# Kernel optimization log

Measured on AMD Instinct MI355X. Metric: run time of the kernel, lower is better.

The kernel has to match this reference:

```python
import jax, jax.numpy as jnp
import numpy as np

B, Q, S, T, H = 8, 64, 64, 64, 768
NH, HD = 12, 64  # head_num, head_dim


def setup_inputs() -> dict:
    key = jax.random.key(0)
    k1, k2, k3, k4, k5, k6, k7 = jax.random.split(key, 7)
    ini_q = jax.random.normal(k1, (B, Q, H), dtype=jnp.float32)
    ini_k = jax.random.normal(k2, (B, S, T, H), dtype=jnp.float32)
    mask = jax.random.randint(k3, (B, S, T), 0, 2).astype(jnp.float32)  # 1 = masked
    # learned params (Linear weights stored as [in, out] for x @ W)
    sc = 1.0 / np.sqrt(H)
    Wq = jax.random.normal(k4, (H, H), dtype=jnp.float32) * sc
    Wkv = jax.random.normal(k5, (H, H), dtype=jnp.float32) * sc
    Wo = jax.random.normal(k6, (H, H), dtype=jnp.float32) * sc
    bo = jax.random.normal(k7, (H,), dtype=jnp.float32) * 0.02
    return {"ini_q": ini_q, "ini_k": ini_k, "mask": mask,
            "Wq": Wq, "Wkv": Wkv, "Wo": Wo, "bo": bo}


def reference(ini_q, ini_k, mask, Wq, Wkv, Wo, bo):
    batch, q_num, _ = ini_q.shape
    _, s_num, t_num, _ = ini_k.shape
    scale = 1.0 / np.sqrt(HD)
    q = (ini_q @ Wq).reshape(batch, q_num, NH, HD)
    kv = (ini_k @ Wkv).reshape(batch, s_num, t_num, NH, HD)  # k == v
    # [b, h, q, s, t]
    scores = jnp.einsum('bqhd,bsthd->bhqst', q, kv) * scale
    scores = scores + mask[:, None, None, :, :] * -10000.0
    alpha = jax.nn.softmax(scores, axis=4)  # dropout is identity in eval
    res = jnp.einsum('bhqst,bsthd->bqshd', alpha, kv).reshape(batch, q_num, s_num, NH * HD)
    return res @ Wo + bo
```

## Files before the change

### kernel.cpp

```cpp
#include <hip/hip_runtime.h>
#include <stdint.h>


typedef __bf16 bf16_t;
typedef __attribute__((ext_vector_type(8))) __bf16 bf16x8;
typedef __attribute__((ext_vector_type(4))) __bf16 bf16x4;
typedef __attribute__((ext_vector_type(4))) float f32x4;

#define HDIM 768

__device__ __forceinline__ void gload16(const bf16_t* g, bf16_t* l) {
  __builtin_amdgcn_global_load_lds(
      (const __attribute__((address_space(1))) void*)g,
      (__attribute__((address_space(3))) void*)l, 16, 0, 0);
}

__global__ __launch_bounds__(256) void split4_kernel(const float* __restrict__ x,
                                                     bf16_t* __restrict__ h,
                                                     bf16_t* __restrict__ l) {
  const int i = blockIdx.x * 256 + threadIdx.x;
  const float4 v = ((const float4*)x)[i];
  const float vv[4] = {v.x, v.y, v.z, v.w};
  bf16x4 hv, lv;
#pragma unroll
  for (int e = 0; e < 4; ++e) {
    const bf16_t hb = (bf16_t)vv[e];
    hv[e] = hb;
    lv[e] = (bf16_t)(vv[e] - (float)hb);
  }
  ((bf16x4*)h)[i] = hv;
  ((bf16x4*)l)[i] = lv;
}

__global__ __launch_bounds__(256) void splitT3_kernel(
    const float* __restrict__ W0, const float* __restrict__ W1,
    const float* __restrict__ W2,
    bf16_t* __restrict__ h0, bf16_t* __restrict__ l0,
    bf16_t* __restrict__ h1, bf16_t* __restrict__ l1,
    bf16_t* __restrict__ h2, bf16_t* __restrict__ l2) {
  const int kt = blockIdx.x * 64, nt = blockIdx.y * 64, ws = blockIdx.z;
  const float* W = ws == 0 ? W0 : (ws == 1 ? W1 : W2);
  bf16_t* H = ws == 0 ? h0 : (ws == 1 ? h1 : h2);
  bf16_t* L = ws == 0 ? l0 : (ws == 1 ? l1 : l2);
  __shared__ bf16_t Th[64 * 72], Tl[64 * 72];
  const int tid = threadIdx.x;
  const int r0 = tid >> 4, c0 = (tid & 15) * 4;
#pragma unroll
  for (int rg = 0; rg < 4; ++rg) {
    const int r = r0 + rg * 16;
    const float4 v = *(const float4*)&W[(size_t)(kt + r) * HDIM + nt + c0];
    const float vv[4] = {v.x, v.y, v.z, v.w};
#pragma unroll
    for (int e = 0; e < 4; ++e) {
      const bf16_t hb = (bf16_t)vv[e];
      Th[(c0 + e) * 72 + r] = hb;
      Tl[(c0 + e) * 72 + r] = (bf16_t)(vv[e] - (float)hb);
    }
  }
  __syncthreads();
  const int n = tid >> 2, kc = (tid & 3) * 16;
  bf16x8 oh[2], ol[2];
#pragma unroll
  for (int e = 0; e < 16; ++e) {
    oh[e >> 3][e & 7] = Th[n * 72 + kc + e];
    ol[e >> 3][e & 7] = Tl[n * 72 + kc + e];
  }
  const size_t ob = (size_t)(nt + n) * HDIM + kt + kc;
  *(bf16x8*)&H[ob] = oh[0];
  *(bf16x8*)&H[ob + 8] = oh[1];
  *(bf16x8*)&L[ob] = ol[0];
  *(bf16x8*)&L[ob + 8] = ol[1];
}

template <int EPI>
__global__ __launch_bounds__(256) void gemm_kernel(
    const bf16_t* __restrict__ Agh, const bf16_t* __restrict__ Agl,
    const bf16_t* __restrict__ Bgh, const bf16_t* __restrict__ Bgl,
    bf16_t* __restrict__ Ch, bf16_t* __restrict__ Cl,
    bf16_t* __restrict__ CNh, bf16_t* __restrict__ CNl,
    float* __restrict__ Cf, const float* __restrict__ bias) {
  __shared__ bf16_t sA[2][2][128 * 32];
  __shared__ bf16_t sB[2][2][128 * 32];
  const int nwg = gridDim.x;
  const int cpx = nwg >> 3;
  const int g = blockIdx.x;
  const int wg = (g & 7) * cpx + (g >> 3);
  const int bn = wg % 6, bm = wg / 6;
  const int tid = threadIdx.x, lane = tid & 63, w = tid >> 6;
  const int wr = (w >> 1) * 64, wc = (w & 1) * 64;
  const int l15 = lane & 15, l4 = lane >> 4;
  f32x4 acc[4][4] = {};

  auto stage = [&](int buf, int kt) {
    const int k0 = kt * 32;
#pragma unroll
    for (int j = 0; j < 2; ++j) {
      const int c0 = j * 256 + w * 64;
      const int c = c0 + lane;
      const int row = c >> 2, slot = c & 3;
      const int soff = ((slot ^ ((row >> 1) & 3)) * 8);
      const size_t ga = (size_t)(bm * 128 + row) * HDIM + k0 + soff;
      gload16(&Agh[ga], &sA[buf][0][c0 * 8]);
      gload16(&Agl[ga], &sA[buf][1][c0 * 8]);
      const size_t gb = (size_t)(bn * 128 + row) * HDIM + k0 + soff;
      gload16(&Bgh[gb], &sB[buf][0][c0 * 8]);
      gload16(&Bgl[gb], &sB[buf][1][c0 * 8]);
    }
  };

  stage(0, 0);
  __syncthreads();
  int cur = 0;

  for (int kt = 0; kt < 24; ++kt) {
    if (kt < 23) stage(cur ^ 1, kt + 1);
    bf16x8 a_h[4], a_l[4], b_h[4], b_l[4];
#pragma unroll
    for (int m = 0; m < 4; ++m) {
      const int rowa = wr + m * 16 + l15;
      const int ra = rowa * 32 + ((l4 ^ ((rowa >> 1) & 3)) * 8);
      a_h[m] = *(const bf16x8*)&sA[cur][0][ra];
      a_l[m] = *(const bf16x8*)&sA[cur][1][ra];
      const int rowb = wc + m * 16 + l15;
      const int rb = rowb * 32 + ((l4 ^ ((rowb >> 1) & 3)) * 8);
      b_h[m] = *(const bf16x8*)&sB[cur][0][rb];
      b_l[m] = *(const bf16x8*)&sB[cur][1][rb];
    }
#pragma unroll
    for (int m = 0; m < 4; ++m)
#pragma unroll
      for (int n = 0; n < 4; ++n) {
        acc[m][n] = __builtin_amdgcn_mfma_f32_16x16x32_bf16(a_h[m], b_h[n], acc[m][n], 0, 0, 0);
        acc[m][n] = __builtin_amdgcn_mfma_f32_16x16x32_bf16(a_h[m], b_l[n], acc[m][n], 0, 0, 0);
        acc[m][n] = __builtin_amdgcn_mfma_f32_16x16x32_bf16(a_l[m], b_h[n], acc[m][n], 0, 0, 0);
      }
    __syncthreads();
    cur ^= 1;
  }

#pragma unroll
  for (int m = 0; m < 4; ++m)
#pragma unroll
    for (int n = 0; n < 4; ++n) {
      const int row0 = bm * 128 + wr + m * 16 + l4 * 4;
      const int col = bn * 128 + wc + n * 16 + l15;
      if constexpr (EPI == 1) {
        const float bv = bias[col];
#pragma unroll
        for (int j = 0; j < 4; ++j)
          Cf[(size_t)(row0 + j) * HDIM + col] = acc[m][n][j] + bv;
      } else if constexpr (EPI == 0) {
#pragma unroll
        for (int j = 0; j < 4; ++j) {
          const float v = acc[m][n][j];
          const bf16_t hb = (bf16_t)v;
          Ch[(size_t)(row0 + j) * HDIM + col] = hb;
          Cl[(size_t)(row0 + j) * HDIM + col] = (bf16_t)(v - (float)hb);
        }
      } else {
        const int b = row0 >> 12, s = (row0 >> 6) & 63, t0 = row0 & 63;
        const int hh = col >> 6, d = col & 63;
        const size_t base = ((size_t)((b * 64 + s) * 12 + hh)) * 4096;
#pragma unroll
        for (int j = 0; j < 4; ++j) {
          const float v = acc[m][n][j];
          const bf16_t hb = (bf16_t)v;
          CNh[base + (t0 + j) * 64 + d] = hb;
          CNl[base + (t0 + j) * 64 + d] = (bf16_t)(v - (float)hb);
        }
      }
    }
}

__global__ __launch_bounds__(256, 3) void attn_kernel(
    const bf16_t* __restrict__ qh, const bf16_t* __restrict__ ql,
    const bf16_t* __restrict__ kvNh, const bf16_t* __restrict__ kvNl,
    const float* __restrict__ mask,
    bf16_t* __restrict__ resh, bf16_t* __restrict__ resl) {
  const int sq = blockIdx.x, hh = blockIdx.y, b = blockIdx.z;
  const int s0 = sq * 8;
  const int tid = threadIdx.x, lane = tid & 63, w = tid >> 6;
  const int l15 = lane & 15, l4 = lane >> 4;
  __shared__ bf16_t Kh[64 * 64], Kl[64 * 64];
  __shared__ bf16_t VTh[64 * 72], VTl[64 * 72];
  __shared__ bf16_t Ph[64 * 68], Pl[64 * 68];
  __shared__ float mk[8 * 64];

  {
    const int i2 = tid * 2;
    const float2 mv = *(const float2*)
        &mask[((size_t)(b * 64 + s0 + (i2 >> 6))) * 64 + (i2 & 63)];
    mk[i2] = mv.x * -10000.0f;
    mk[i2 + 1] = mv.y * -10000.0f;
  }

  const size_t qbase = ((size_t)(b * 64 + w * 16 + l15)) * HDIM + hh * 64;
  bf16x8 qf_h[2], qf_l[2];
#pragma unroll
  for (int ks = 0; ks < 2; ++ks) {
    qf_h[ks] = *(const bf16x8*)&qh[qbase + ks * 32 + l4 * 8];
    qf_l[ks] = *(const bf16x8*)&ql[qbase + ks * 32 + l4 * 8];
  }

  const size_t hb0 = ((size_t)((b * 64 + s0) * 12 + hh)) * 4096;
  const size_t SSTR = 12 * 4096;

  bf16x8 nxh[2], nxl[2];
  auto load_next = [&](int sn) {
#pragma unroll
    for (int j = 0; j < 2; ++j) {
      const int c = j * 256 + tid;
      const size_t src = hb0 + (size_t)sn * SSTR + (c >> 3) * 64 + (c & 7) * 8;
      nxh[j] = *(const bf16x8*)&kvNh[src];
      nxl[j] = *(const bf16x8*)&kvNl[src];
    }
  };
  auto write_K = [&]() {
#pragma unroll
    for (int j = 0; j < 2; ++j) {
      const int c = j * 256 + tid;
      const int t = c >> 3, sl = c & 7;
      const int off = t * 64 + ((sl ^ (t & 7)) * 8);
      *(bf16x8*)&Kh[off] = nxh[j];
      *(bf16x8*)&Kl[off] = nxl[j];
    }
  };

  load_next(0);
  write_K();
  __syncthreads();

  const int q = w * 16 + l15;
  for (int si = 0; si < 8; ++si) {
    if (si < 7) load_next(si + 1);

    f32x4 St[4] = {};
#pragma unroll
    for (int ks = 0; ks < 2; ++ks) {
#pragma unroll
      for (int mf = 0; mf < 4; ++mf) {
        const int t = mf * 16 + l15;
        const int off = t * 64 + (((ks * 4 + l4) ^ (t & 7)) * 8);
        const bf16x8 kh8 = *(const bf16x8*)&Kh[off];
        const bf16x8 kl8 = *(const bf16x8*)&Kl[off];
        St[mf] = __builtin_amdgcn_mfma_f32_16x16x32_bf16(kh8, qf_h[ks], St[mf], 0, 0, 0);
        St[mf] = __builtin_amdgcn_mfma_f32_16x16x32_bf16(kh8, qf_l[ks], St[mf], 0, 0, 0);
        St[mf] = __builtin_amdgcn_mfma_f32_16x16x32_bf16(kl8, qf_h[ks], St[mf], 0, 0, 0);
      }
    }

    {
      const int t = lane, sw = t & 7;
#pragma unroll
      for (int ri = 0; ri < 2; ++ri) {
        const int phys = (w * 2 + ri) ^ sw;
        const bf16x8 vh = *(const bf16x8*)&Kh[t * 64 + phys * 8];
        const bf16x8 vl = *(const bf16x8*)&Kl[t * 64 + phys * 8];
        const int d0 = w * 16 + ri * 8;
#pragma unroll
        for (int e = 0; e < 8; ++e) {
          VTh[(d0 + e) * 72 + t] = vh[e];
          VTl[(d0 + e) * 72 + t] = vl[e];
        }
      }
    }

    float p[16];
    float mx = -1e30f;
#pragma unroll
    for (int mf = 0; mf < 4; ++mf)
#pragma unroll
      for (int j = 0; j < 4; ++j) {
        const float v = St[mf][j] * 0.125f + mk[si * 64 + mf * 16 + l4 * 4 + j];
        p[mf * 4 + j] = v;
        mx = fmaxf(mx, v);
      }
    mx = fmaxf(mx, __shfl_xor(mx, 16));
    mx = fmaxf(mx, __shfl_xor(mx, 32));
    float sum = 0.f;
#pragma unroll
    for (int i = 0; i < 16; ++i) {
      const float e = __expf(p[i] - mx);
      p[i] = e;
      sum += e;
    }
    sum += __shfl_xor(sum, 16);
    sum += __shfl_xor(sum, 32);
    const float inv = 1.0f / sum;

#pragma unroll
    for (int mf = 0; mf < 4; ++mf) {
      bf16x4 hv, lv;
#pragma unroll
      for (int j = 0; j < 4; ++j) {
        const float v = p[mf * 4 + j] * inv;
        const bf16_t hb = (bf16_t)v;
        hv[j] = hb;
        lv[j] = (bf16_t)(v - (float)hb);
      }
      *(bf16x4*)&Ph[q * 68 + mf * 16 + l4 * 4] = hv;
      *(bf16x4*)&Pl[q * 68 + mf * 16 + l4 * 4] = lv;
    }
    __syncthreads();

    if (si < 7) write_K();

    f32x4 O[4] = {};
#pragma unroll
    for (int ks = 0; ks < 2; ++ks) {
      const bf16x8 pa = *(const bf16x8*)&Ph[q * 68 + ks * 32 + l4 * 8];
      const bf16x8 pb = *(const bf16x8*)&Pl[q * 68 + ks * 32 + l4 * 8];
#pragma unroll
      for (int nf = 0; nf < 4; ++nf) {
        const int d = nf * 16 + l15;
        const bf16x8 vh = *(const bf16x8*)&VTh[d * 72 + ks * 32 + l4 * 8];
        const bf16x8 vl = *(const bf16x8*)&VTl[d * 72 + ks * 32 + l4 * 8];
        O[nf] = __builtin_amdgcn_mfma_f32_16x16x32_bf16(pa, vh, O[nf], 0, 0, 0);
        O[nf] = __builtin_amdgcn_mfma_f32_16x16x32_bf16(pa, vl, O[nf], 0, 0, 0);
        O[nf] = __builtin_amdgcn_mfma_f32_16x16x32_bf16(pb, vh, O[nf], 0, 0, 0);
      }
    }

#pragma unroll
    for (int nf = 0; nf < 4; ++nf)
#pragma unroll
      for (int j = 0; j < 4; ++j) {
        const int qo = w * 16 + l4 * 4 + j;
        const size_t idx =
            ((size_t)((b * 64 + qo) * 64 + s0 + si)) * HDIM + hh * 64 + nf * 16 + l15;
        const float v = O[nf][j];
        const bf16_t hb = (bf16_t)v;
        resh[idx] = hb;
        resl[idx] = (bf16_t)(v - (float)hb);
      }
    __syncthreads();
  }
}

extern "C" void kernel_launch(void* const* d_in, const int* in_sizes, int n_in,
                              void* d_out, int out_size, void* d_ws, size_t ws_size,
                              hipStream_t stream) {
  const float* ini_q = (const float*)d_in[0];
  const float* ini_k = (const float*)d_in[1];
  const float* mask = (const float*)d_in[2];
  const float* Wq = (const float*)d_in[3];
  const float* Wkv = (const float*)d_in[4];
  const float* Wo = (const float*)d_in[5];
  const float* bo = (const float*)d_in[6];
  float* out = (float*)d_out;

  const size_t SQ = 512ull * HDIM;
  const size_t SK = 32768ull * HDIM;
  const size_t SW = 768ull * HDIM;

  char* p = (char*)d_ws;
  auto carve = [&](size_t bytes) {
    char* r = p;
    p += (bytes + 255) & ~(size_t)255;
    return r;
  };
  bf16_t* iq_h = (bf16_t*)carve(SQ * 2);
  bf16_t* iq_l = (bf16_t*)carve(SQ * 2);
  bf16_t* ik_h = (bf16_t*)carve(SK * 2);
  bf16_t* ik_l = (bf16_t*)carve(SK * 2);
  bf16_t* wq_h = (bf16_t*)carve(SW * 2);
  bf16_t* wq_l = (bf16_t*)carve(SW * 2);
  bf16_t* wkv_h = (bf16_t*)carve(SW * 2);
  bf16_t* wkv_l = (bf16_t*)carve(SW * 2);
  bf16_t* wo_h = (bf16_t*)carve(SW * 2);
  bf16_t* wo_l = (bf16_t*)carve(SW * 2);
  bf16_t* q_h = (bf16_t*)carve(SQ * 2);
  bf16_t* q_l = (bf16_t*)carve(SQ * 2);
  bf16_t* kvN_h = (bf16_t*)carve(SK * 2);
  bf16_t* kvN_l = (bf16_t*)carve(SK * 2);
  bf16_t* res_h = ik_h;
  bf16_t* res_l = ik_l;
  if ((size_t)(p - (char*)d_ws) > ws_size) return;

  split4_kernel<<<dim3(SQ / 4 / 256), 256, 0, stream>>>(ini_q, iq_h, iq_l);
  split4_kernel<<<dim3(SK / 4 / 256), 256, 0, stream>>>(ini_k, ik_h, ik_l);
  splitT3_kernel<<<dim3(12, 12, 3), 256, 0, stream>>>(
      Wq, Wkv, Wo, wq_h, wq_l, wkv_h, wkv_l, wo_h, wo_l);

  gemm_kernel<0><<<dim3(24), 256, 0, stream>>>(
      iq_h, iq_l, wq_h, wq_l, q_h, q_l, nullptr, nullptr, nullptr, nullptr);
  gemm_kernel<2><<<dim3(1536), 256, 0, stream>>>(
      ik_h, ik_l, wkv_h, wkv_l, nullptr, nullptr, kvN_h, kvN_l, nullptr, nullptr);
  attn_kernel<<<dim3(8, 12, 8), 256, 0, stream>>>(
      q_h, q_l, kvN_h, kvN_l, mask, res_h, res_l);
  gemm_kernel<1><<<dim3(1536), 256, 0, stream>>>(
      res_h, res_l, wo_h, wo_l, nullptr, nullptr, nullptr, nullptr, out, bo);
}
```

Measured before the change: 543.8 us.

## Single-buffer GEMM, stage bf16 epilogue in LDS, drop head-major KV layout

```diff
diff --git a/kernel.cpp b/kernel.cpp
--- a/kernel.cpp
+++ b/kernel.cpp
@@ -77,10 +77,12 @@
     const bf16_t* __restrict__ Agh, const bf16_t* __restrict__ Agl,
     const bf16_t* __restrict__ Bgh, const bf16_t* __restrict__ Bgl,
     bf16_t* __restrict__ Ch, bf16_t* __restrict__ Cl,
-    bf16_t* __restrict__ CNh, bf16_t* __restrict__ CNl,
     float* __restrict__ Cf, const float* __restrict__ bias) {
-  __shared__ bf16_t sA[2][2][128 * 32];
-  __shared__ bf16_t sB[2][2][128 * 32];
+  __shared__ bf16_t SM[4][128 * 32];
+  bf16_t* sAh = SM[0];
+  bf16_t* sAl = SM[1];
+  bf16_t* sBh = SM[2];
+  bf16_t* sBl = SM[3];
   const int nwg = gridDim.x;
   const int cpx = nwg >> 3;
   const int g = blockIdx.x;
@@ -91,8 +93,9 @@
   const int l15 = lane & 15, l4 = lane >> 4;
   f32x4 acc[4][4] = {};
 
-  auto stage = [&](int buf, int kt) {
+  for (int kt = 0; kt < 24; ++kt) {
     const int k0 = kt * 32;
+    __syncthreads();
 #pragma unroll
     for (int j = 0; j < 2; ++j) {
       const int c0 = j * 256 + w * 64;
@@ -100,31 +103,24 @@
       const int row = c >> 2, slot = c & 3;
       const int soff = ((slot ^ ((row >> 1) & 3)) * 8);
       const size_t ga = (size_t)(bm * 128 + row) * HDIM + k0 + soff;
-      gload16(&Agh[ga], &sA[buf][0][c0 * 8]);
-      gload16(&Agl[ga], &sA[buf][1][c0 * 8]);
+      gload16(&Agh[ga], &sAh[c0 * 8]);
+      gload16(&Agl[ga], &sAl[c0 * 8]);
       const size_t gb = (size_t)(bn * 128 + row) * HDIM + k0 + soff;
-      gload16(&Bgh[gb], &sB[buf][0][c0 * 8]);
-      gload16(&Bgl[gb], &sB[buf][1][c0 * 8]);
-    }
-  };
-
-  stage(0, 0);
-  __syncthreads();
-  int cur = 0;
-
-  for (int kt = 0; kt < 24; ++kt) {
-    if (kt < 23) stage(cur ^ 1, kt + 1);
+      gload16(&Bgh[gb], &sBh[c0 * 8]);
+      gload16(&Bgl[gb], &sBl[c0 * 8]);
+    }
+    __syncthreads();
     bf16x8 a_h[4], a_l[4], b_h[4], b_l[4];
 #pragma unroll
     for (int m = 0; m < 4; ++m) {
       const int rowa = wr + m * 16 + l15;
       const int ra = rowa * 32 + ((l4 ^ ((rowa >> 1) & 3)) * 8);
-      a_h[m] = *(const bf16x8*)&sA[cur][0][ra];
-      a_l[m] = *(const bf16x8*)&sA[cur][1][ra];
+      a_h[m] = *(const bf16x8*)&sAh[ra];
+      a_l[m] = *(const bf16x8*)&sAl[ra];
       const int rowb = wc + m * 16 + l15;
       const int rb = rowb * 32 + ((l4 ^ ((rowb >> 1) & 3)) * 8);
-      b_h[m] = *(const bf16x8*)&sB[cur][0][rb];
-      b_l[m] = *(const bf16x8*)&sB[cur][1][rb];
+      b_h[m] = *(const bf16x8*)&sBh[rb];
+      b_l[m] = *(const bf16x8*)&sBl[rb];
     }
 #pragma unroll
     for (int m = 0; m < 4; ++m)
@@ -134,47 +130,59 @@
         acc[m][n] = __builtin_amdgcn_mfma_f32_16x16x32_bf16(a_h[m], b_l[n], acc[m][n], 0, 0, 0);
         acc[m][n] = __builtin_amdgcn_mfma_f32_16x16x32_bf16(a_l[m], b_h[n], acc[m][n], 0, 0, 0);
       }
-    __syncthreads();
-    cur ^= 1;
-  }
-
-#pragma unroll
-  for (int m = 0; m < 4; ++m)
-#pragma unroll
-    for (int n = 0; n < 4; ++n) {
-      const int row0 = bm * 128 + wr + m * 16 + l4 * 4;
-      const int col = bn * 128 + wc + n * 16 + l15;
-      if constexpr (EPI == 1) {
+  }
+
+  if constexpr (EPI == 1) {
+#pragma unroll
+    for (int m = 0; m < 4; ++m)
+#pragma unroll
+      for (int n = 0; n < 4; ++n) {
+        const int row0 = bm * 128 + wr + m * 16 + l4 * 4;
+        const int col = bn * 128 + wc + n * 16 + l15;
         const float bv = bias[col];
 #pragma unroll
         for (int j = 0; j < 4; ++j)
           Cf[(size_t)(row0 + j) * HDIM + col] = acc[m][n][j] + bv;
-      } else if constexpr (EPI == 0) {
-#pragma unroll
-        for (int j = 0; j < 4; ++j) {
-          const float v = acc[m][n][j];
-          const bf16_t hb = (bf16_t)v;
-          Ch[(size_t)(row0 + j) * HDIM + col] = hb;
-          Cl[(size_t)(row0 + j) * HDIM + col] = (bf16_t)(v - (float)hb);
+      }
+  } else {
+    bf16_t* CW = SM[0];
+    __syncthreads();
+#pragma unroll
+    for (int pass = 0; pass < 2; ++pass) {
+#pragma unroll
+      for (int m = 0; m < 4; ++m)
+#pragma unroll
+        for (int n = 0; n < 4; ++n) {
+#pragma unroll
+          for (int j = 0; j < 4; ++j) {
+            const int r = wr + m * 16 + l4 * 4 + j;
+            const int c = wc + n * 16 + l15;
+            const int slot = c >> 3;
+            const int phys = (slot & 12) | ((slot & 3) ^ ((r >> 2) & 3));
+            const float v = acc[m][n][j];
+            const bf16_t hb = (bf16_t)v;
+            CW[r * 128 + phys * 8 + (c & 7)] =
+                pass == 0 ? hb : (bf16_t)(v - (float)hb);
+          }
         }
-      } else {
-        const int b = row0 >> 12, s = (row0 >> 6) & 63, t0 = row0 & 63;
-        const int hh = col >> 6, d = col & 63;
-        const size_t base = ((size_t)((b * 64 + s) * 12 + hh)) * 4096;
-#pragma unroll
-        for (int j = 0; j < 4; ++j) {
-          const float v = acc[m][n][j];
-          const bf16_t hb = (bf16_t)v;
-          CNh[base + (t0 + j) * 64 + d] = hb;
-          CNl[base + (t0 + j) * 64 + d] = (bf16_t)(v - (float)hb);
-        }
-      }
-    }
+      __syncthreads();
+      bf16_t* dst = pass == 0 ? Ch : Cl;
+#pragma unroll
+      for (int it = 0; it < 8; ++it) {
+        const int idx = it * 256 + tid;
+        const int r = idx >> 4, slot = idx & 15;
+        const int phys = (slot & 12) | ((slot & 3) ^ ((r >> 2) & 3));
+        const bf16x8 v8 = *(const bf16x8*)&CW[r * 128 + phys * 8];
+        *(bf16x8*)&dst[(size_t)(bm * 128 + r) * HDIM + bn * 128 + slot * 8] = v8;
+      }
+      if (pass == 0) __syncthreads();
+    }
+  }
 }
 
 __global__ __launch_bounds__(256, 3) void attn_kernel(
     const bf16_t* __restrict__ qh, const bf16_t* __restrict__ ql,
-    const bf16_t* __restrict__ kvNh, const bf16_t* __restrict__ kvNl,
+    const bf16_t* __restrict__ kvh, const bf16_t* __restrict__ kvl,
     const float* __restrict__ mask,
     bf16_t* __restrict__ resh, bf16_t* __restrict__ resl) {
   const int sq = blockIdx.x, hh = blockIdx.y, b = blockIdx.z;
@@ -202,17 +210,17 @@
     qf_l[ks] = *(const bf16x8*)&ql[qbase + ks * 32 + l4 * 8];
   }
 
-  const size_t hb0 = ((size_t)((b * 64 + s0) * 12 + hh)) * 4096;
-  const size_t SSTR = 12 * 4096;
+  const size_t kv0 = ((size_t)(b * 4096 + s0 * 64)) * HDIM + hh * 64;
+  const size_t SSTR = (size_t)64 * HDIM;
 
   bf16x8 nxh[2], nxl[2];
   auto load_next = [&](int sn) {
 #pragma unroll
     for (int j = 0; j < 2; ++j) {
       const int c = j * 256 + tid;
-      const size_t src = hb0 + (size_t)sn * SSTR + (c >> 3) * 64 + (c & 7) * 8;
-      nxh[j] = *(const bf16x8*)&kvNh[src];
-      nxl[j] = *(const bf16x8*)&kvNl[src];
+      const size_t src = kv0 + (size_t)sn * SSTR + (size_t)(c >> 3) * HDIM + (c & 7) * 8;
+      nxh[j] = *(const bf16x8*)&kvh[src];
+      nxl[j] = *(const bf16x8*)&kvl[src];
     }
   };
   auto write_K = [&]() {
@@ -235,6 +243,7 @@
     if (si < 7) load_next(si + 1);
 
     f32x4 St[4] = {};
+    __builtin_amdgcn_s_setprio(1);
 #pragma unroll
     for (int ks = 0; ks < 2; ++ks) {
 #pragma unroll
@@ -248,6 +257,7 @@
         St[mf] = __builtin_amdgcn_mfma_f32_16x16x32_bf16(kl8, qf_h[ks], St[mf], 0, 0, 0);
       }
     }
+    __builtin_amdgcn_s_setprio(0);
 
     {
       const int t = lane, sw = t & 7;
@@ -306,6 +316,7 @@
     if (si < 7) write_K();
 
     f32x4 O[4] = {};
+    __builtin_amdgcn_s_setprio(1);
 #pragma unroll
     for (int ks = 0; ks < 2; ++ks) {
       const bf16x8 pa = *(const bf16x8*)&Ph[q * 68 + ks * 32 + l4 * 8];
@@ -320,19 +331,32 @@
         O[nf] = __builtin_amdgcn_mfma_f32_16x16x32_bf16(pb, vh, O[nf], 0, 0, 0);
       }
     }
+    __builtin_amdgcn_s_setprio(0);
 
 #pragma unroll
     for (int nf = 0; nf < 4; ++nf)
 #pragma unroll
       for (int j = 0; j < 4; ++j) {
-        const int qo = w * 16 + l4 * 4 + j;
-        const size_t idx =
-            ((size_t)((b * 64 + qo) * 64 + s0 + si)) * HDIM + hh * 64 + nf * 16 + l15;
+        const int r = w * 16 + l4 * 4 + j;
+        const int d = nf * 16 + l15;
         const float v = O[nf][j];
         const bf16_t hb = (bf16_t)v;
-        resh[idx] = hb;
-        resl[idx] = (bf16_t)(v - (float)hb);
-      }
+        Ph[r * 68 + d] = hb;
+        Pl[r * 68 + d] = (bf16_t)(v - (float)hb);
+      }
+    {
+      const int q2 = w * 16 + (lane >> 2), ch = lane & 3;
+      const bf16x8 h8a = *(const bf16x8*)&Ph[q2 * 68 + ch * 16];
+      const bf16x8 h8b = *(const bf16x8*)&Ph[q2 * 68 + ch * 16 + 8];
+      const bf16x8 l8a = *(const bf16x8*)&Pl[q2 * 68 + ch * 16];
+      const bf16x8 l8b = *(const bf16x8*)&Pl[q2 * 68 + ch * 16 + 8];
+      const size_t idx =
+          ((size_t)((b * 64 + q2) * 64 + s0 + si)) * HDIM + hh * 64 + ch * 16;
+      *(bf16x8*)&resh[idx] = h8a;
+      *(bf16x8*)&resh[idx + 8] = h8b;
+      *(bf16x8*)&resl[idx] = l8a;
+      *(bf16x8*)&resl[idx + 8] = l8b;
+    }
     __syncthreads();
   }
 }
@@ -371,8 +395,8 @@
   bf16_t* wo_l = (bf16_t*)carve(SW * 2);
   bf16_t* q_h = (bf16_t*)carve(SQ * 2);
   bf16_t* q_l = (bf16_t*)carve(SQ * 2);
-  bf16_t* kvN_h = (bf16_t*)carve(SK * 2);
-  bf16_t* kvN_l = (bf16_t*)carve(SK * 2);
+  bf16_t* kv_h = (bf16_t*)carve(SK * 2);
+  bf16_t* kv_l = (bf16_t*)carve(SK * 2);
   bf16_t* res_h = ik_h;
   bf16_t* res_l = ik_l;
   if ((size_t)(p - (char*)d_ws) > ws_size) return;
@@ -383,11 +407,11 @@
       Wq, Wkv, Wo, wq_h, wq_l, wkv_h, wkv_l, wo_h, wo_l);
 
   gemm_kernel<0><<<dim3(24), 256, 0, stream>>>(
-      iq_h, iq_l, wq_h, wq_l, q_h, q_l, nullptr, nullptr, nullptr, nullptr);
-  gemm_kernel<2><<<dim3(1536), 256, 0, stream>>>(
-      ik_h, ik_l, wkv_h, wkv_l, nullptr, nullptr, kvN_h, kvN_l, nullptr, nullptr);
+      iq_h, iq_l, wq_h, wq_l, q_h, q_l, nullptr, nullptr);
+  gemm_kernel<0><<<dim3(1536), 256, 0, stream>>>(
+      ik_h, ik_l, wkv_h, wkv_l, kv_h, kv_l, nullptr, nullptr);
   attn_kernel<<<dim3(8, 12, 8), 256, 0, stream>>>(
-      q_h, q_l, kvN_h, kvN_l, mask, res_h, res_l);
+      q_h, q_l, kv_h, kv_l, mask, res_h, res_l);
   gemm_kernel<1><<<dim3(1536), 256, 0, stream>>>(
-      res_h, res_l, wo_h, wo_l, nullptr, nullptr, nullptr, nullptr, out, bo);
-}
+      res_h, res_l, wo_h, wo_l, nullptr, nullptr, out, bo);
+}
```

New measurement: 513.5 us. 5.6% less time.
